# Kernel tuning notes

Measured on AMD Instinct MI355X. Metric: run time of the kernel, lower is better.

## Reference

```python
import jax, jax.numpy as jnp
import numpy as np

B, T, D_IN = 16, 4096, 512
D_EMB, K = 256, 1024


def setup_inputs() -> dict:
    key = jax.random.key(0)
    k1, k2, k3, k4 = jax.random.split(key, 4)
    z_e = jax.random.normal(k1, (B, T, D_IN), dtype=jnp.float32)
    # nn.Embedding default init: N(0,1)
    codebook = jax.random.normal(k2, (K, D_EMB), dtype=jnp.float32)
    # nn.Linear(bias=False) weights, [out, in]
    W_down = jax.random.normal(k3, (D_EMB, D_IN), dtype=jnp.float32) / np.sqrt(D_IN)
    W_up = jax.random.normal(k4, (D_IN, D_EMB), dtype=jnp.float32) / np.sqrt(D_EMB)
    return {"z_e": z_e, "codebook": codebook, "W_down": W_down, "W_up": W_up}


def reference(z_e, codebook, W_down, W_up):
    # proj down: [B,T,D_IN] -> [B,T,D_EMB]
    z_e_down = jnp.einsum('btd,ed->bte', z_e, W_down)
    zf = z_e_down.reshape(-1, z_e_down.shape[-1])  # [BT, D_EMB]
    # squared L2 distances: ||z||^2 - 2 z.C^T + ||c||^2
    dist = (jnp.sum(zf * zf, axis=1, keepdims=True)
            - 2.0 * zf @ codebook.T
            + jnp.sum(codebook * codebook, axis=1)[None, :])  # [BT, K]
    code = jnp.argmin(dist, axis=1).reshape(z_e.shape[0], z_e.shape[1])  # [B, T]
    z_q_down = jnp.take(codebook, code, axis=0)  # [B, T, D_EMB]
    # training (freeze=False) path: VQ losses + straight-through estimator
    sq = (z_q_down - z_e_down) ** 2
    commitment_loss = jnp.mean(sq, axis=(1, 2))  # [B] (grad to z_e_down in torch)
    codebook_loss = jnp.mean(sq, axis=(1, 2))    # [B] (grad to codebook in torch)
    z_q_down_ste = z_e_down + jax.lax.stop_gradient(z_q_down - z_e_down)
    z_q = jnp.einsum('bte,de->btd', z_q_down_ste, W_up)  # [B, T, D_IN]
    return z_q, z_e_down, code, commitment_loss, codebook_loss
```

## Files before the change

### kernel.cpp

```cpp
#include <hip/hip_runtime.h>
#include <math.h>

#define BT_TOTAL 65536
#define DIN 512
#define DEMB 256
#define KCODES 1024

typedef __attribute__((ext_vector_type(8))) short short8;
typedef __attribute__((ext_vector_type(4))) float floatx4;
typedef __attribute__((ext_vector_type(16))) float floatx16;

__device__ __forceinline__ unsigned short f2bf(float x) {
    unsigned u = __float_as_uint(x);
    unsigned r = u + 0x7fffu + ((u >> 16) & 1u);
    return (unsigned short)(r >> 16);
}
__device__ __forceinline__ float bf2f(unsigned short h) {
    return __uint_as_float(((unsigned)h) << 16);
}

__global__ __launch_bounds__(256) void cnorm_kernel(const float* __restrict__ cbook,
                                                    float* __restrict__ cnorm,
                                                    float* __restrict__ out_loss) {
    const int k = blockIdx.x;
    const int tid = threadIdx.x;
    float v = cbook[k * DEMB + tid];
    v *= v;
#pragma unroll
    for (int o = 32; o > 0; o >>= 1) v += __shfl_down(v, o);
    __shared__ float ps[4];
    if ((tid & 63) == 0) ps[tid >> 6] = v;
    __syncthreads();
    if (tid == 0) cnorm[k] = ps[0] + ps[1] + ps[2] + ps[3];
    if (k == 0 && tid < 32) out_loss[tid] = 0.0f;
}

__global__ __launch_bounds__(256) void swz32_kernel(const float* __restrict__ Bt,
                                                    unsigned short* __restrict__ hi,
                                                    unsigned short* __restrict__ lo,
                                                    int K, int total) {
    const int o = blockIdx.x * 256 + threadIdx.x;
    if (o >= total) return;
    const int j = o & 7;
    const int l = (o >> 3) & 63;
    const int r = o >> 9;
    const int kst = K >> 4;
    const int s = r % kst;
    const int t = r / kst;
    const int c = t * 32 + (l & 31);
    const int k = s * 16 + (l >> 5) * 8 + j;
    const float v = Bt[(size_t)c * K + k];
    const unsigned short h = f2bf(v);
    hi[o] = (unsigned short)h;
    lo[o] = f2bf(v - bf2f(h));
}

template <int KD, int NSTR>
__global__ __launch_bounds__(256) void gemm_rowdot(const float* __restrict__ A,
                                                   const float* __restrict__ Bt,
                                                   float* __restrict__ C) {
    __shared__ __align__(16) float As[64][36];
    __shared__ __align__(16) float Bs[64][36];
    const int tid = threadIdx.x;
    const int tx = tid & 15, ty = tid >> 4;
    const int rowBase = blockIdx.x * 64;
    const int colBase = blockIdx.y * 64;
    const int lr = tid >> 2;
    const int lk = (tid & 3) * 8;
    float acc[4][4] = {};
    for (int k0 = 0; k0 < KD; k0 += 32) {
        const float4 a0 = *(const float4*)(A + (size_t)(rowBase + lr) * KD + k0 + lk);
        const float4 a1 = *(const float4*)(A + (size_t)(rowBase + lr) * KD + k0 + lk + 4);
        const float4 b0 = *(const float4*)(Bt + (size_t)(colBase + lr) * KD + k0 + lk);
        const float4 b1 = *(const float4*)(Bt + (size_t)(colBase + lr) * KD + k0 + lk + 4);
        __syncthreads();
        *(float4*)&As[lr][lk] = a0;
        *(float4*)&As[lr][lk + 4] = a1;
        *(float4*)&Bs[lr][lk] = b0;
        *(float4*)&Bs[lr][lk + 4] = b1;
        __syncthreads();
#pragma unroll
        for (int e = 0; e < 32; e += 4) {
            float4 va[4], vb[4];
#pragma unroll
            for (int i = 0; i < 4; ++i) va[i] = *(const float4*)&As[4 * ty + i][e];
#pragma unroll
            for (int j = 0; j < 4; ++j) vb[j] = *(const float4*)&Bs[4 * tx + j][e];
#pragma unroll
            for (int i = 0; i < 4; ++i)
#pragma unroll
                for (int j = 0; j < 4; ++j) {
                    acc[i][j] = fmaf(va[i].x, vb[j].x, acc[i][j]);
                    acc[i][j] = fmaf(va[i].y, vb[j].y, acc[i][j]);
                    acc[i][j] = fmaf(va[i].z, vb[j].z, acc[i][j]);
                    acc[i][j] = fmaf(va[i].w, vb[j].w, acc[i][j]);
                }
        }
    }
#pragma unroll
    for (int i = 0; i < 4; ++i) {
        float4 o = make_float4(acc[i][0], acc[i][1], acc[i][2], acc[i][3]);
        *(float4*)(C + (size_t)(rowBase + 4 * ty + i) * NSTR + colBase + 4 * tx) = o;
    }
}

__global__ __launch_bounds__(128, 2) void gemm_down_mfma(const float* __restrict__ A,
                                                         const unsigned short* __restrict__ bhi,
                                                         const unsigned short* __restrict__ blo,
                                                         float* __restrict__ C) {
    __shared__ __align__(16) short lds_h[2][8][512];
    __shared__ __align__(16) short lds_l[2][8][512];
    const int tid = threadIdx.x;
    const int lane = tid & 63, wv = tid >> 6;
    const int cc = lane & 31, half = lane >> 5;
    const int rowBase = blockIdx.x * 64 + wv * 32;

    floatx16 acc[8];
#pragma unroll
    for (int t = 0; t < 8; ++t)
#pragma unroll
        for (int r = 0; r < 16; ++r) acc[t][r] = 0.f;

    const float* arow = A + (size_t)(rowBase + cc) * DIN + half * 8;

    short8 ach, acl;
    {
        const float4 a0 = *(const float4*)(arow);
        const float4 a1 = *(const float4*)(arow + 4);
        const float xs[8] = {a0.x, a0.y, a0.z, a0.w, a1.x, a1.y, a1.z, a1.w};
#pragma unroll
        for (int j = 0; j < 8; ++j) {
            const unsigned short h = f2bf(xs[j]);
            ach[j] = (short)h;
            acl[j] = (short)f2bf(xs[j] - bf2f(h));
        }
    }
#pragma unroll
    for (int i = 0; i < 8; ++i) {
        const int c = wv * 8 + i;
        const int t = c >> 1;
        const unsigned short* src = (c & 1) ? blo : bhi;
        const short8 vst = *(const short8*)(src + ((size_t)(t * 32) * 64 + lane) * 8);
        short* dst = (c & 1) ? &lds_l[0][t][lane * 8] : &lds_h[0][t][lane * 8];
        *(short8*)dst = vst;
    }
    __syncthreads();

    int buf = 0;
    for (int s = 0; s < 32; ++s) {
        short8 pf[8];
        float4 av0, av1;
        if (s < 31) {
#pragma unroll
            for (int i = 0; i < 8; ++i) {
                const int c = wv * 8 + i;
                const int t = c >> 1;
                const unsigned short* src = (c & 1) ? blo : bhi;
                pf[i] = *(const short8*)(src + ((size_t)(t * 32 + s + 1) * 64 + lane) * 8);
            }
            av0 = *(const float4*)(arow + (s + 1) * 16);
            av1 = *(const float4*)(arow + (s + 1) * 16 + 4);
        }
        __builtin_amdgcn_s_setprio(1);
#pragma unroll
        for (int t = 0; t < 8; ++t) {
            const short8 bh = *(const short8*)&lds_h[buf][t][lane * 8];
            const short8 bl = *(const short8*)&lds_l[buf][t][lane * 8];
            acc[t] = __builtin_amdgcn_mfma_f32_32x32x16_bf16(ach, bh, acc[t], 0, 0, 0);
            acc[t] = __builtin_amdgcn_mfma_f32_32x32x16_bf16(acl, bh, acc[t], 0, 0, 0);
            acc[t] = __builtin_amdgcn_mfma_f32_32x32x16_bf16(ach, bl, acc[t], 0, 0, 0);
        }
        __builtin_amdgcn_s_setprio(0);
        if (s < 31) {
            const float xs[8] = {av0.x, av0.y, av0.z, av0.w, av1.x, av1.y, av1.z, av1.w};
#pragma unroll
            for (int j = 0; j < 8; ++j) {
                const unsigned short h = f2bf(xs[j]);
                ach[j] = (short)h;
                acl[j] = (short)f2bf(xs[j] - bf2f(h));
            }
#pragma unroll
            for (int i = 0; i < 8; ++i) {
                const int c = wv * 8 + i;
                const int t = c >> 1;
                short* dst = (c & 1) ? &lds_l[buf ^ 1][t][lane * 8]
                                     : &lds_h[buf ^ 1][t][lane * 8];
                *(short8*)dst = pf[i];
            }
        }
        __syncthreads();
        buf ^= 1;
    }
#pragma unroll
    for (int t = 0; t < 8; ++t)
#pragma unroll
        for (int r = 0; r < 16; ++r) {
            const int row = (r & 3) + 8 * (r >> 2) + 4 * half;
            C[(size_t)(rowBase + row) * DEMB + t * 32 + cc] = acc[t][r];
        }
}

#define DIST_CHUNKS(BASE)                                                                     \
    {                                                                                         \
        _Pragma("unroll") for (int s8 = 0; s8 < 8; s8 += 2) {                                 \
            const short8 bh0 = *(const short8*)&lds_h[buf][s8][lane * 8];                     \
            const short8 bl0 = *(const short8*)&lds_l[buf][s8][lane * 8];                     \
            const short8 bh1 = *(const short8*)&lds_h[buf][s8 + 1][lane * 8];                 \
            const short8 bl1 = *(const short8*)&lds_l[buf][s8 + 1][lane * 8];                 \
            accA = __builtin_amdgcn_mfma_f32_32x32x16_bf16(ahi[BASE + s8], bh0, accA, 0, 0, 0);     \
            accB = __builtin_amdgcn_mfma_f32_32x32x16_bf16(ahi[BASE + s8 + 1], bh1, accB, 0, 0, 0); \
            accA = __builtin_amdgcn_mfma_f32_32x32x16_bf16(alo[BASE + s8], bh0, accA, 0, 0, 0);     \
            accB = __builtin_amdgcn_mfma_f32_32x32x16_bf16(alo[BASE + s8 + 1], bh1, accB, 0, 0, 0); \
            accA = __builtin_amdgcn_mfma_f32_32x32x16_bf16(ahi[BASE + s8], bl0, accA, 0, 0, 0);     \
            accB = __builtin_amdgcn_mfma_f32_32x32x16_bf16(ahi[BASE + s8 + 1], bl1, accB, 0, 0, 0); \
        }                                                                                     \
    }

__global__ __launch_bounds__(128, 2) void dist_mfma(const float* __restrict__ zed,
                                                    const unsigned short* __restrict__ chi,
                                                    const unsigned short* __restrict__ clo,
                                                    const float* __restrict__ cnorm,
                                                    float* __restrict__ out_code,
                                                    float* __restrict__ out_loss) {
    __shared__ __align__(16) short lds_h[2][8][512];
    __shared__ __align__(16) short lds_l[2][8][512];
    __shared__ float cn_s[KCODES];
    __shared__ float znorm_s[2][32];
    const int tid = threadIdx.x;
    const int lane = tid & 63, wv = tid >> 6;
    const int cc = lane & 31, half = lane >> 5;
    const int rowBase = blockIdx.x * 64 + wv * 32;

    *(float4*)&cn_s[tid * 8] = *(const float4*)(cnorm + tid * 8);
    *(float4*)&cn_s[tid * 8 + 4] = *(const float4*)(cnorm + tid * 8 + 4);

    short8 ahi[16], alo[16];
    float zn = 0.f;
    const float* arow = zed + (size_t)(rowBase + cc) * DEMB + half * 8;
#pragma unroll
    for (int s = 0; s < 16; ++s) {
        const float4 v0 = *(const float4*)(arow + s * 16);
        const float4 v1 = *(const float4*)(arow + s * 16 + 4);
        const float xs[8] = {v0.x, v0.y, v0.z, v0.w, v1.x, v1.y, v1.z, v1.w};
#pragma unroll
        for (int j = 0; j < 8; ++j) {
            const unsigned short h = f2bf(xs[j]);
            ahi[s][j] = (short)h;
            alo[s][j] = (short)f2bf(xs[j] - bf2f(h));
            zn = fmaf(xs[j], xs[j], zn);
        }
    }
    zn += __shfl_xor(zn, 32, 64);
    if (half == 0) znorm_s[wv][cc] = zn;

#pragma unroll
    for (int i = 0; i < 8; ++i) {
        const int c = wv * 8 + i;
        const int s8 = c >> 1;
        const unsigned short* src = (c & 1) ? clo : chi;
        const short8 vst = *(const short8*)(src + ((size_t)s8 * 64 + lane) * 8);
        short* dst = (c & 1) ? &lds_l[0][s8][lane * 8] : &lds_h[0][s8][lane * 8];
        *(short8*)dst = vst;
    }
    __syncthreads();

    floatx16 accA, accB;
    float bestv[16];
    int besti[16];
#pragma unroll
    for (int r = 0; r < 16; ++r) {
        accA[r] = 0.f;
        accB[r] = 0.f;
        bestv[r] = INFINITY;
        besti[r] = 0;
    }
    int buf = 0;

    for (int ph = 0; ph < 64; ++ph) {
        const int t = ph >> 1;
        short8 pf[8];
        if (ph < 63) {
            const int tn = (ph + 1) >> 1;
            const int sb = ((ph + 1) & 1) * 8;
#pragma unroll
            for (int i = 0; i < 8; ++i) {
                const int c = wv * 8 + i;
                const int s8 = c >> 1;
                const unsigned short* src = (c & 1) ? clo : chi;
                pf[i] = *(const short8*)(src + ((size_t)(tn * 16 + sb + s8) * 64 + lane) * 8);
            }
        }
        __builtin_amdgcn_s_setprio(1);
        if ((ph & 1) == 0) {
            DIST_CHUNKS(0)
        } else {
            DIST_CHUNKS(8)
        }
        __builtin_amdgcn_s_setprio(0);
        if (ph & 1) {
            const float cn = cn_s[t * 32 + cc];
            const int code = t * 32 + cc;
#pragma unroll
            for (int r = 0; r < 16; ++r) {
                const float d = fmaf(-2.f, accA[r] + accB[r], cn);
                if (d < bestv[r]) {
                    bestv[r] = d;
                    besti[r] = code;
                }
                accA[r] = 0.f;
                accB[r] = 0.f;
            }
        }
        if (ph < 63) {
#pragma unroll
            for (int i = 0; i < 8; ++i) {
                const int c = wv * 8 + i;
                const int s8 = c >> 1;
                short* dst = (c & 1) ? &lds_l[buf ^ 1][s8][lane * 8]
                                     : &lds_h[buf ^ 1][s8][lane * 8];
                *(short8*)dst = pf[i];
            }
        }
        __syncthreads();
        buf ^= 1;
    }

#pragma unroll
    for (int off = 1; off < 32; off <<= 1) {
#pragma unroll
        for (int r = 0; r < 16; ++r) {
            const float ov = __shfl_xor(bestv[r], off, 64);
            const int oi = __shfl_xor(besti[r], off, 64);
            if (ov < bestv[r] || (ov == bestv[r] && oi < besti[r])) {
                bestv[r] = ov;
                besti[r] = oi;
            }
        }
    }
    float ls = 0.f;
    if (cc == 0) {
#pragma unroll
        for (int r = 0; r < 16; ++r) {
            const int row = (r & 3) + 8 * (r >> 2) + 4 * half;
            out_code[rowBase + row] = (float)besti[r];
            ls += bestv[r] + znorm_s[wv][row];
        }
    }
    ls += __shfl_xor(ls, 32, 64);
    if (lane == 0) {
        const int b = blockIdx.x >> 6;
        const float val = ls * (1.0f / (4096.0f * 256.0f));
        atomicAdd(&out_loss[b], val);
        atomicAdd(&out_loss[16 + b], val);
    }
}

__global__ __launch_bounds__(256) void gather_kernel(const float* __restrict__ P,
                                                     const float* __restrict__ code_f,
                                                     float* __restrict__ zq) {
    const int lane = threadIdx.x & 63;
    const int row = blockIdx.x * 4 + (threadIdx.x >> 6);
    const int c = (int)code_f[row];
    const float4* src = (const float4*)(P + (size_t)c * DIN);
    float4* dst = (float4*)(zq + (size_t)row * DIN);
    dst[lane] = src[lane];
    dst[lane + 64] = src[lane + 64];
}

extern "C" void kernel_launch(void* const* d_in, const int* in_sizes, int n_in,
                              void* d_out, int out_size, void* d_ws, size_t ws_size,
                              hipStream_t stream) {
    const float* z_e = (const float*)d_in[0];
    const float* cbook = (const float*)d_in[1];
    const float* W_down = (const float*)d_in[2];
    const float* W_up = (const float*)d_in[3];

    float* out = (float*)d_out;
    float* out_zq = out;
    float* out_zed = out + 33554432;
    float* out_code = out_zed + 16777216;
    float* out_loss = out_code + 65536;

    char* wsb = (char*)d_ws;
    float* cnorm = (float*)wsb;
    unsigned short* cb_hi = (unsigned short*)(wsb + 4096);
    unsigned short* cb_lo = (unsigned short*)(wsb + 4096 + 524288);
    unsigned short* wd_hi = (unsigned short*)(wsb + 4096 + 2 * 524288);
    unsigned short* wd_lo = (unsigned short*)(wsb + 4096 + 2 * 524288 + 262144);
    float* P = (float*)(wsb + 4096);

    cnorm_kernel<<<KCODES, 256, 0, stream>>>(cbook, cnorm, out_loss);
    swz32_kernel<<<1024, 256, 0, stream>>>(cbook, cb_hi, cb_lo, 256, 262144);
    swz32_kernel<<<512, 256, 0, stream>>>(W_down, wd_hi, wd_lo, 512, 131072);

    gemm_down_mfma<<<BT_TOTAL / 64, 128, 0, stream>>>(z_e, wd_hi, wd_lo, out_zed);
    dist_mfma<<<BT_TOTAL / 64, 128, 0, stream>>>(out_zed, cb_hi, cb_lo, cnorm,
                                                 out_code, out_loss);
    gemm_rowdot<256, 512><<<dim3(16, 8), 256, 0, stream>>>(cbook, W_up, P);
    gather_kernel<<<BT_TOTAL / 4, 256, 0, stream>>>(P, out_code, out_zq);
}
```

Baseline: 536.6 us.

## Double block size to 4 waves and deepen K-stage per barrier in MFMA kernels

Both the down-projection GEMM and the distance kernel now run 256-thread blocks covering 128 rows. Each shared-memory codebook or weight stage is reused by four waves instead of two. Each pipeline stage also processes twice as much K (two 16-wide chunks, or a full 32-code tile in dist), which halves the number of barriers. The loss reduction now goes through an LDS atomic per block, so there are fewer global atomics. The cost is larger LDS footprint and more registers per stage, which may reduce occupancy.

```diff
diff --git a/kernel.cpp b/kernel.cpp
--- a/kernel.cpp
+++ b/kernel.cpp
@@ -104,16 +104,16 @@
     }
 }
 
-__global__ __launch_bounds__(128, 2) void gemm_down_mfma(const float* __restrict__ A,
+__global__ __launch_bounds__(256, 2) void gemm_down_mfma(const float* __restrict__ A,
                                                          const unsigned short* __restrict__ bhi,
                                                          const unsigned short* __restrict__ blo,
                                                          float* __restrict__ C) {
-    __shared__ __align__(16) short lds_h[2][8][512];
-    __shared__ __align__(16) short lds_l[2][8][512];
+    __shared__ __align__(16) short lds_h[2][2][8][512];
+    __shared__ __align__(16) short lds_l[2][2][8][512];
     const int tid = threadIdx.x;
     const int lane = tid & 63, wv = tid >> 6;
     const int cc = lane & 31, half = lane >> 5;
-    const int rowBase = blockIdx.x * 64 + wv * 32;
+    const int rowBase = blockIdx.x * 128 + wv * 32;
 
     floatx16 acc[8];
 #pragma unroll
@@ -123,68 +123,88 @@
 
     const float* arow = A + (size_t)(rowBase + cc) * DIN + half * 8;
 
-    short8 ach, acl;
+    short8 ach[2], acl[2];
     {
-        const float4 a0 = *(const float4*)(arow);
-        const float4 a1 = *(const float4*)(arow + 4);
-        const float xs[8] = {a0.x, a0.y, a0.z, a0.w, a1.x, a1.y, a1.z, a1.w};
-#pragma unroll
-        for (int j = 0; j < 8; ++j) {
-            const unsigned short h = f2bf(xs[j]);
-            ach[j] = (short)h;
-            acl[j] = (short)f2bf(xs[j] - bf2f(h));
-        }
+        const float4 a00 = *(const float4*)(arow);
+        const float4 a01 = *(const float4*)(arow + 4);
+        const float4 a10 = *(const float4*)(arow + 16);
+        const float4 a11 = *(const float4*)(arow + 20);
+        const float xs[16] = {a00.x, a00.y, a00.z, a00.w, a01.x, a01.y, a01.z, a01.w,
+                              a10.x, a10.y, a10.z, a10.w, a11.x, a11.y, a11.z, a11.w};
+#pragma unroll
+        for (int kc = 0; kc < 2; ++kc)
+#pragma unroll
+            for (int j = 0; j < 8; ++j) {
+                const float x = xs[kc * 8 + j];
+                const unsigned short h = f2bf(x);
+                ach[kc][j] = (short)h;
+                acl[kc][j] = (short)f2bf(x - bf2f(h));
+            }
     }
 #pragma unroll
     for (int i = 0; i < 8; ++i) {
         const int c = wv * 8 + i;
-        const int t = c >> 1;
+        const int t = c >> 2;
+        const int kc = (c >> 1) & 1;
         const unsigned short* src = (c & 1) ? blo : bhi;
-        const short8 vst = *(const short8*)(src + ((size_t)(t * 32) * 64 + lane) * 8);
-        short* dst = (c & 1) ? &lds_l[0][t][lane * 8] : &lds_h[0][t][lane * 8];
+        const short8 vst = *(const short8*)(src + ((size_t)(t * 32 + kc) * 64 + lane) * 8);
+        short* dst = (c & 1) ? &lds_l[0][kc][t][lane * 8] : &lds_h[0][kc][t][lane * 8];
         *(short8*)dst = vst;
     }
     __syncthreads();
 
     int buf = 0;
-    for (int s = 0; s < 32; ++s) {
+    for (int p = 0; p < 16; ++p) {
         short8 pf[8];
-        float4 av0, av1;
-        if (s < 31) {
+        float4 av[4];
+        if (p < 15) {
 #pragma unroll
             for (int i = 0; i < 8; ++i) {
                 const int c = wv * 8 + i;
-                const int t = c >> 1;
+                const int t = c >> 2;
+                const int kc = (c >> 1) & 1;
                 const unsigned short* src = (c & 1) ? blo : bhi;
-                pf[i] = *(const short8*)(src + ((size_t)(t * 32 + s + 1) * 64 + lane) * 8);
-            }
-            av0 = *(const float4*)(arow + (s + 1) * 16);
-            av1 = *(const float4*)(arow + (s + 1) * 16 + 4);
+                pf[i] = *(const short8*)(src +
+                                         ((size_t)(t * 32 + (p + 1) * 2 + kc) * 64 + lane) * 8);
+            }
+            av[0] = *(const float4*)(arow + (p + 1) * 32);
+            av[1] = *(const float4*)(arow + (p + 1) * 32 + 4);
+            av[2] = *(const float4*)(arow + (p + 1) * 32 + 16);
+            av[3] = *(const float4*)(arow + (p + 1) * 32 + 20);
         }
         __builtin_amdgcn_s_setprio(1);
 #pragma unroll
-        for (int t = 0; t < 8; ++t) {
-            const short8 bh = *(const short8*)&lds_h[buf][t][lane * 8];
-            const short8 bl = *(const short8*)&lds_l[buf][t][lane * 8];
-            acc[t] = __builtin_amdgcn_mfma_f32_32x32x16_bf16(ach, bh, acc[t], 0, 0, 0);
-            acc[t] = __builtin_amdgcn_mfma_f32_32x32x16_bf16(acl, bh, acc[t], 0, 0, 0);
-            acc[t] = __builtin_amdgcn_mfma_f32_32x32x16_bf16(ach, bl, acc[t], 0, 0, 0);
-        }
+        for (int kc = 0; kc < 2; ++kc)
+#pragma unroll
+            for (int t = 0; t < 8; ++t) {
+                const short8 bh = *(const short8*)&lds_h[buf][kc][t][lane * 8];
+                const short8 bl = *(const short8*)&lds_l[buf][kc][t][lane * 8];
+                acc[t] = __builtin_amdgcn_mfma_f32_32x32x16_bf16(ach[kc], bh, acc[t], 0, 0, 0);
+                acc[t] = __builtin_amdgcn_mfma_f32_32x32x16_bf16(acl[kc], bh, acc[t], 0, 0, 0);
+                acc[t] = __builtin_amdgcn_mfma_f32_32x32x16_bf16(ach[kc], bl, acc[t], 0, 0, 0);
+            }
         __builtin_amdgcn_s_setprio(0);
-        if (s < 31) {
-            const float xs[8] = {av0.x, av0.y, av0.z, av0.w, av1.x, av1.y, av1.z, av1.w};
-#pragma unroll
-            for (int j = 0; j < 8; ++j) {
-                const unsigned short h = f2bf(xs[j]);
-                ach[j] = (short)h;
-                acl[j] = (short)f2bf(xs[j] - bf2f(h));
-            }
+        if (p < 15) {
+            const float xs[16] = {av[0].x, av[0].y, av[0].z, av[0].w,
+                                  av[1].x, av[1].y, av[1].z, av[1].w,
+                                  av[2].x, av[2].y, av[2].z, av[2].w,
+                                  av[3].x, av[3].y, av[3].z, av[3].w};
+#pragma unroll
+            for (int kc = 0; kc < 2; ++kc)
+#pragma unroll
+                for (int j = 0; j < 8; ++j) {
+                    const float x = xs[kc * 8 + j];
+                    const unsigned short h = f2bf(x);
+                    ach[kc][j] = (short)h;
+                    acl[kc][j] = (short)f2bf(x - bf2f(h));
+                }
 #pragma unroll
             for (int i = 0; i < 8; ++i) {
                 const int c = wv * 8 + i;
-                const int t = c >> 1;
-                short* dst = (c & 1) ? &lds_l[buf ^ 1][t][lane * 8]
-                                     : &lds_h[buf ^ 1][t][lane * 8];
+                const int t = c >> 2;
+                const int kc = (c >> 1) & 1;
+                short* dst = (c & 1) ? &lds_l[buf ^ 1][kc][t][lane * 8]
+                                     : &lds_h[buf ^ 1][kc][t][lane * 8];
                 *(short8*)dst = pf[i];
             }
         }
@@ -200,39 +220,24 @@
         }
 }
 
-#define DIST_CHUNKS(BASE)                                                                     \
-    {                                                                                         \
-        _Pragma("unroll") for (int s8 = 0; s8 < 8; s8 += 2) {                                 \
-            const short8 bh0 = *(const short8*)&lds_h[buf][s8][lane * 8];                     \
-            const short8 bl0 = *(const short8*)&lds_l[buf][s8][lane * 8];                     \
-            const short8 bh1 = *(const short8*)&lds_h[buf][s8 + 1][lane * 8];                 \
-            const short8 bl1 = *(const short8*)&lds_l[buf][s8 + 1][lane * 8];                 \
-            accA = __builtin_amdgcn_mfma_f32_32x32x16_bf16(ahi[BASE + s8], bh0, accA, 0, 0, 0);     \
-            accB = __builtin_amdgcn_mfma_f32_32x32x16_bf16(ahi[BASE + s8 + 1], bh1, accB, 0, 0, 0); \
-            accA = __builtin_amdgcn_mfma_f32_32x32x16_bf16(alo[BASE + s8], bh0, accA, 0, 0, 0);     \
-            accB = __builtin_amdgcn_mfma_f32_32x32x16_bf16(alo[BASE + s8 + 1], bh1, accB, 0, 0, 0); \
-            accA = __builtin_amdgcn_mfma_f32_32x32x16_bf16(ahi[BASE + s8], bl0, accA, 0, 0, 0);     \
-            accB = __builtin_amdgcn_mfma_f32_32x32x16_bf16(ahi[BASE + s8 + 1], bl1, accB, 0, 0, 0); \
-        }                                                                                     \
-    }
-
-__global__ __launch_bounds__(128, 2) void dist_mfma(const float* __restrict__ zed,
+__global__ __launch_bounds__(256, 2) void dist_mfma(const float* __restrict__ zed,
                                                     const unsigned short* __restrict__ chi,
                                                     const unsigned short* __restrict__ clo,
                                                     const float* __restrict__ cnorm,
                                                     float* __restrict__ out_code,
                                                     float* __restrict__ out_loss) {
-    __shared__ __align__(16) short lds_h[2][8][512];
-    __shared__ __align__(16) short lds_l[2][8][512];
+    __shared__ __align__(16) short lds_h[2][16][512];
+    __shared__ __align__(16) short lds_l[2][16][512];
     __shared__ float cn_s[KCODES];
-    __shared__ float znorm_s[2][32];
+    __shared__ float znorm_s[4][32];
+    __shared__ float blockSum;
     const int tid = threadIdx.x;
     const int lane = tid & 63, wv = tid >> 6;
     const int cc = lane & 31, half = lane >> 5;
-    const int rowBase = blockIdx.x * 64 + wv * 32;
-
-    *(float4*)&cn_s[tid * 8] = *(const float4*)(cnorm + tid * 8);
-    *(float4*)&cn_s[tid * 8 + 4] = *(const float4*)(cnorm + tid * 8 + 4);
+    const int rowBase = blockIdx.x * 128 + wv * 32;
+
+    *(float4*)&cn_s[tid * 4] = *(const float4*)(cnorm + tid * 4);
+    if (tid == 0) blockSum = 0.f;
 
     short8 ahi[16], alo[16];
     float zn = 0.f;
@@ -276,28 +281,33 @@
     }
     int buf = 0;
 
-    for (int ph = 0; ph < 64; ++ph) {
-        const int t = ph >> 1;
+    for (int t = 0; t < 32; ++t) {
         short8 pf[8];
-        if (ph < 63) {
-            const int tn = (ph + 1) >> 1;
-            const int sb = ((ph + 1) & 1) * 8;
+        if (t < 31) {
 #pragma unroll
             for (int i = 0; i < 8; ++i) {
                 const int c = wv * 8 + i;
                 const int s8 = c >> 1;
                 const unsigned short* src = (c & 1) ? clo : chi;
-                pf[i] = *(const short8*)(src + ((size_t)(tn * 16 + sb + s8) * 64 + lane) * 8);
+                pf[i] = *(const short8*)(src + ((size_t)((t + 1) * 16 + s8) * 64 + lane) * 8);
             }
         }
         __builtin_amdgcn_s_setprio(1);
-        if ((ph & 1) == 0) {
-            DIST_CHUNKS(0)
-        } else {
-            DIST_CHUNKS(8)
+#pragma unroll
+        for (int s8 = 0; s8 < 16; s8 += 2) {
+            const short8 bh0 = *(const short8*)&lds_h[buf][s8][lane * 8];
+            const short8 bl0 = *(const short8*)&lds_l[buf][s8][lane * 8];
+            const short8 bh1 = *(const short8*)&lds_h[buf][s8 + 1][lane * 8];
+            const short8 bl1 = *(const short8*)&lds_l[buf][s8 + 1][lane * 8];
+            accA = __builtin_amdgcn_mfma_f32_32x32x16_bf16(ahi[s8], bh0, accA, 0, 0, 0);
+            accB = __builtin_amdgcn_mfma_f32_32x32x16_bf16(ahi[s8 + 1], bh1, accB, 0, 0, 0);
+            accA = __builtin_amdgcn_mfma_f32_32x32x16_bf16(alo[s8], bh0, accA, 0, 0, 0);
+            accB = __builtin_amdgcn_mfma_f32_32x32x16_bf16(alo[s8 + 1], bh1, accB, 0, 0, 0);
+            accA = __builtin_amdgcn_mfma_f32_32x32x16_bf16(ahi[s8], bl0, accA, 0, 0, 0);
+            accB = __builtin_amdgcn_mfma_f32_32x32x16_bf16(ahi[s8 + 1], bl1, accB, 0, 0, 0);
         }
         __builtin_amdgcn_s_setprio(0);
-        if (ph & 1) {
+        {
             const float cn = cn_s[t * 32 + cc];
             const int code = t * 32 + cc;
 #pragma unroll
@@ -311,7 +321,7 @@
                 accB[r] = 0.f;
             }
         }
-        if (ph < 63) {
+        if (t < 31) {
 #pragma unroll
             for (int i = 0; i < 8; ++i) {
                 const int c = wv * 8 + i;
@@ -337,21 +347,22 @@
             }
         }
     }
-    float ls = 0.f;
     if (cc == 0) {
+        float ls = 0.f;
 #pragma unroll
         for (int r = 0; r < 16; ++r) {
             const int row = (r & 3) + 8 * (r >> 2) + 4 * half;
             out_code[rowBase + row] = (float)besti[r];
             ls += bestv[r] + znorm_s[wv][row];
         }
-    }
-    ls += __shfl_xor(ls, 32, 64);
-    if (lane == 0) {
-        const int b = blockIdx.x >> 6;
-        const float val = ls * (1.0f / (4096.0f * 256.0f));
-        atomicAdd(&out_loss[b], val);
-        atomicAdd(&out_loss[16 + b], val);
+        atomicAdd(&blockSum, ls);
+    }
+    __syncthreads();
+    if (tid == 0) {
+        const int b = blockIdx.x >> 5;
+        const float v = blockSum * (1.0f / (4096.0f * 256.0f));
+        atomicAdd(&out_loss[b], v);
+        atomicAdd(&out_loss[16 + b], v);
     }
 }
 
@@ -393,9 +404,9 @@
     swz32_kernel<<<1024, 256, 0, stream>>>(cbook, cb_hi, cb_lo, 256, 262144);
     swz32_kernel<<<512, 256, 0, stream>>>(W_down, wd_hi, wd_lo, 512, 131072);
 
-    gemm_down_mfma<<<BT_TOTAL / 64, 128, 0, stream>>>(z_e, wd_hi, wd_lo, out_zed);
-    dist_mfma<<<BT_TOTAL / 64, 128, 0, stream>>>(out_zed, cb_hi, cb_lo, cnorm,
-                                                 out_code, out_loss);
+    gemm_down_mfma<<<BT_TOTAL / 128, 256, 0, stream>>>(z_e, wd_hi, wd_lo, out_zed);
+    dist_mfma<<<BT_TOTAL / 128, 256, 0, stream>>>(out_zed, cb_hi, cb_lo, cnorm,
+                                                  out_code, out_loss);
     gemm_rowdot<256, 512><<<dim3(16, 8), 256, 0, stream>>>(cbook, W_up, P);
     gather_kernel<<<BT_TOTAL / 4, 256, 0, stream>>>(P, out_code, out_zq);
 }
```

Result: faster. 458.4 us (-14.6%).
